# Optimization experiments

Measured on AMD Instinct MI355X. Metric: run time of the kernel, lower is better.

The kernel has to match this reference:

```python
import jax, jax.numpy as jnp
import numpy as np

EPS = 1e-20  # MaskSoftmax epsilon
S, T, B, H, V = 64, 64, 128, 1024, 32000


def _attn(s, h, u, mask, sa_w, sa_b, a1_w, a1_b):
    # Bahdanau attention with mask-softmax over the source (dim 0)
    t = jnp.tanh(s @ sa_w + sa_b + u)               # [S,B,H]
    e = jnp.einsum('sbh,h->sb', t, a1_w) + a1_b     # [S,B]
    x = jnp.exp(e - jnp.max(e, axis=0, keepdims=True)) * mask
    alpha = x / (jnp.sum(x, axis=0, keepdims=True) + EPS)
    return jnp.einsum('sb,sbh->bh', alpha, h)       # [B,H]


def _gru(x, h, ym, W, U, b, C=None, c=None):
    xg = x @ W + b
    if C is not None:
        xg = xg + c @ C
    hg = h @ U
    xz, xr, xh = jnp.split(xg, 3, axis=-1)
    hz, hr, hh = jnp.split(hg, 3, axis=-1)
    z = jax.nn.sigmoid(xz + hz)
    r = jax.nn.sigmoid(xr + hr)
    hn = (1.0 - z) * h + z * jnp.tanh(xh + r * hh)
    m = ym[:, None]
    return m * hn + (1.0 - m) * h


def _forward(ys, xs_h, uh, xs_mask, ys_mask, s_tm1, emb, sa_w, sa_b, a1_w, a1_b,
             ha_w, ha_b, W1, U1, b1, W2, U2, C2, b2,
             ua1_w, ua1_b, ua2_w, ua2_b, ls_w, ls_b, ly_w, ly_b, lc_w, lc_b):
    ys_e = emb[ys]                                              # [T,B,H]
    btg_uh = jnp.einsum('sbh,hk->sbk', xs_h, ha_w) + ha_b        # [S,B,H]

    def step(s, inp):
        y_e, ym = inp
        s_above = _gru(y_e, s, ym, W1, U1, b1)                   # gru1
        a1 = _attn(s_above, xs_h, uh, xs_mask, sa_w, sa_b, a1_w, a1_b)
        a2 = _attn(s_above, xs_h, btg_uh, xs_mask, sa_w, sa_b, a1_w, a1_b)
        s_t = _gru(a1, s_above, ym, W2, U2, b2, C2, a2)          # gru2 with extra ctx
        g = jax.nn.sigmoid(a1 @ ua1_w + ua1_b + a2 @ ua2_w + ua2_b)
        att = g * a1 + (1.0 - g) * a2                            # gated fusion
        logit = s_t @ ls_w + ls_b + y_e @ ly_w + ly_b + att @ lc_w + lc_b  # [B,2H]
        logit = jnp.max(logit.reshape(logit.shape[0], -1, 2), axis=-1)     # maxout
        return s_t, logit

    _, logits = jax.lax.scan(step, s_tm1, (ys_e, ys_mask))       # [T,B,H]
    return logits * ys_mask[:, :, None]


def setup_inputs():
    key = jax.random.key(0)
    ks = jax.random.split(key, 20)
    rn = lambda k, sh, s=0.02: jax.random.normal(k, sh, jnp.float32) * s
    inp = {}
    inp['ys'] = jax.random.randint(ks[0], (T, B), 0, V)
    inp['xs_h'] = jax.random.normal(ks[1], (S, B, H), jnp.float32)
    inp['uh'] = jax.random.normal(ks[2], (S, B, H), jnp.float32)
    inp['xs_mask'] = jnp.ones((S, B), jnp.float32)
    inp['ys_mask'] = jnp.ones((T, B), jnp.float32)
    inp['s_tm1'] = rn(ks[3], (B, H), 1.0)
    emb = rn(ks[4], (V, H), 1.0)
    inp['emb'] = emb.at[0].set(0.0)  # padding_idx = 0
    inp['sa_w'] = rn(ks[5], (H, H)); inp['sa_b'] = jnp.zeros((H,), jnp.float32)
    inp['a1_w'] = rn(ks[6], (H,));   inp['a1_b'] = jnp.zeros((), jnp.float32)
    inp['ha_w'] = rn(ks[7], (H, H)); inp['ha_b'] = jnp.zeros((H,), jnp.float32)
    inp['W1'] = rn(ks[8], (H, 3 * H)); inp['U1'] = rn(ks[9], (H, 3 * H)); inp['b1'] = jnp.zeros((3 * H,), jnp.float32)
    inp['W2'] = rn(ks[10], (H, 3 * H)); inp['U2'] = rn(ks[11], (H, 3 * H)); inp['C2'] = rn(ks[12], (H, 3 * H)); inp['b2'] = jnp.zeros((3 * H,), jnp.float32)
    inp['ua1_w'] = rn(ks[13], (H, H)); inp['ua1_b'] = jnp.zeros((H,), jnp.float32)
    inp['ua2_w'] = rn(ks[14], (H, H)); inp['ua2_b'] = jnp.zeros((H,), jnp.float32)
    inp['ls_w'] = rn(ks[15], (H, 2 * H)); inp['ls_b'] = jnp.zeros((2 * H,), jnp.float32)
    inp['ly_w'] = rn(ks[16], (H, 2 * H)); inp['ly_b'] = jnp.zeros((2 * H,), jnp.float32)
    inp['lc_w'] = rn(ks[17], (H, 2 * H)); inp['lc_b'] = jnp.zeros((2 * H,), jnp.float32)
    return inp


def reference(ys, xs_h, uh, xs_mask, ys_mask, s_tm1, emb, sa_w, sa_b, a1_w, a1_b,
              ha_w, ha_b, W1, U1, b1, W2, U2, C2, b2,
              ua1_w, ua1_b, ua2_w, ua2_b, ls_w, ls_b, ly_w, ly_b, lc_w, lc_b):
    return _forward(ys, xs_h, uh, xs_mask, ys_mask, s_tm1, emb, sa_w, sa_b, a1_w, a1_b,
                    ha_w, ha_b, W1, U1, b1, W2, U2, C2, b2,
                    ua1_w, ua1_b, ua2_w, ua2_b, ls_w, ls_b, ly_w, ly_b, lc_w, lc_b)
```

## Files before the change

### kernel.cpp

```cpp
#include <hip/hip_runtime.h>
#include <hip/hip_bf16.h>
#include <cstddef>
#include <cstdint>

#define Sdim 64
#define Tdim 64
#define Bdim 128
#define Hdim 1024
#define H3 3072
#define TB (Tdim * Bdim)
#define SB (Sdim * Bdim)
#define NWG 256

typedef __attribute__((ext_vector_type(4))) float f32x4;
typedef __attribute__((ext_vector_type(8))) short bf16x8;

__device__ __forceinline__ float rcpf(float x) { return __builtin_amdgcn_rcpf(x); }
__device__ __forceinline__ float sigf(float x) { return rcpf(1.0f + __expf(-x)); }
__device__ __forceinline__ float tanh_fast(float x) {
  x = fminf(fmaxf(x, -15.0f), 15.0f);
  float t = __expf(2.0f * x);
  return (t - 1.0f) * rcpf(t + 1.0f);
}
__device__ __forceinline__ float bl(uint32_t u) { return __uint_as_float(u << 16); }
__device__ __forceinline__ float bh(uint32_t u) { return __uint_as_float(u & 0xffff0000u); }
__device__ __forceinline__ float b2f(uint16_t v) { return __uint_as_float((uint32_t)v << 16); }
__device__ __forceinline__ uint16_t f2b(float f) {
  __hip_bfloat16 h = __float2bfloat16(f);
  return *reinterpret_cast<uint16_t*>(&h);
}

__device__ __forceinline__ uint32_t ald32(const void* p) {
  return __hip_atomic_load((const uint32_t*)p, __ATOMIC_RELAXED, __HIP_MEMORY_SCOPE_AGENT);
}
__device__ __forceinline__ unsigned long long ald64(const void* p) {
  return __hip_atomic_load((const unsigned long long*)p, __ATOMIC_RELAXED, __HIP_MEMORY_SCOPE_AGENT);
}
__device__ __forceinline__ void ast32(void* p, uint32_t v) {
  __hip_atomic_store((uint32_t*)p, v, __ATOMIC_RELAXED, __HIP_MEMORY_SCOPE_AGENT);
}
__device__ __forceinline__ void ast64(void* p, unsigned long long v) {
  __hip_atomic_store((unsigned long long*)p, v, __ATOMIC_RELAXED, __HIP_MEMORY_SCOPE_AGENT);
}
__device__ __forceinline__ float aldf(const void* p) { return __uint_as_float(ald32(p)); }
__device__ __forceinline__ void astf(void* p, float v) { ast32(p, __float_as_uint(v)); }
__device__ __forceinline__ uint4 ald128(const void* p) {
  unsigned long long a = ald64(p);
  unsigned long long b = ald64((const char*)p + 8);
  uint4 r;
  r.x = (uint32_t)a; r.y = (uint32_t)(a >> 32);
  r.z = (uint32_t)b; r.w = (uint32_t)(b >> 32);
  return r;
}
#define PK2(x, y) ((unsigned long long)__float_as_uint(x) | ((unsigned long long)__float_as_uint(y) << 32))
__device__ __forceinline__ float ulo(unsigned long long u) { return __uint_as_float((uint32_t)u); }
__device__ __forceinline__ float uhi(unsigned long long u) { return __uint_as_float((uint32_t)(u >> 32)); }

struct MDesc {
  const uint16_t* A0; const uint16_t* B0;
  const uint16_t* A1; const uint16_t* B1;
  const uint16_t* A2; const uint16_t* B2;
  const float* bias0; const float* bias1; const float* bias2;
  float* C;
  int M, N, K;
};

template<int BM, int BN, int MODE>
__global__ __launch_bounds__(256) void mgemm(MDesc d, const float* __restrict__ ymask,
                                             float* __restrict__ outp)
{
  const int nb = blockIdx.x * BN;
  const int mb = blockIdx.y * BM;
  if (nb >= d.N || mb >= d.M) return;

  __shared__ char lds[(BM + BN) * 128];
  char* As = lds;
  char* Bs = lds + BM * 128;

  const int t = threadIdx.x;
  const int lane = t & 63;
  const int wid = t >> 6;
  const int wm = wid >> 1, wn = wid & 1;
  constexpr int WM = BM / 2, WN = BN / 2;
  constexpr int MR = WM / 16, NR = WN / 16;
  constexpr int CA = BM / 32;
  constexpr int CB = BN / 32;

  const int arow_base = wm * WM + (lane & 15);
  const int brow_base = wn * WN + (lane & 15);
  const int akb = (lane >> 4) * 16;
  const int axA = (arow_base & 7) << 4;
  const int axB = (brow_base & 7) << 4;

  f32x4 acc[MR][NR];
  #pragma unroll
  for (int m = 0; m < MR; ++m)
    #pragma unroll
    for (int n = 0; n < NR; ++n)
      acc[m][n] = (f32x4){0.f, 0.f, 0.f, 0.f};

  const int K = d.K;
  const int nkt = K / 64;

  #pragma unroll 1
  for (int p = 0; p < 3; ++p) {
    const uint16_t* A = (p == 0) ? d.A0 : (p == 1 ? d.A1 : d.A2);
    const uint16_t* B = (p == 0) ? d.B0 : (p == 1 ? d.B1 : d.B2);
    if (A == nullptr) break;

    const char* gA[CA]; int lA[CA];
    const char* gB[CB]; int lB[CB];
    #pragma unroll
    for (int c = 0; c < CA; ++c) {
      int i = c * 256 + t, row = i >> 3, kb = (i & 7) * 16;
      gA[c] = (const char*)A + (size_t)(mb + row) * K * 2 + kb;
      lA[c] = row * 128 + (kb ^ ((row & 7) << 4));
    }
    #pragma unroll
    for (int c = 0; c < CB; ++c) {
      int i = c * 256 + t, row = i >> 3, kb = (i & 7) * 16;
      gB[c] = (const char*)B + (size_t)(nb + row) * K * 2 + kb;
      lB[c] = row * 128 + (kb ^ ((row & 7) << 4));
    }

    uint4 ra[CA], rb[CB];
    #pragma unroll
    for (int c = 0; c < CA; ++c) ra[c] = *(const uint4*)gA[c];
    #pragma unroll
    for (int c = 0; c < CB; ++c) rb[c] = *(const uint4*)gB[c];

    for (int kk = 0; kk < nkt; ++kk) {
      __syncthreads();
      #pragma unroll
      for (int c = 0; c < CA; ++c) *(uint4*)(As + lA[c]) = ra[c];
      #pragma unroll
      for (int c = 0; c < CB; ++c) *(uint4*)(Bs + lB[c]) = rb[c];
      __syncthreads();
      if (kk + 1 < nkt) {
        #pragma unroll
        for (int c = 0; c < CA; ++c) ra[c] = *(const uint4*)(gA[c] + (size_t)(kk + 1) * 128);
        #pragma unroll
        for (int c = 0; c < CB; ++c) rb[c] = *(const uint4*)(gB[c] + (size_t)(kk + 1) * 128);
      }
      #pragma unroll
      for (int ks = 0; ks < 2; ++ks) {
        bf16x8 av[MR], bv[NR];
        #pragma unroll
        for (int m = 0; m < MR; ++m) {
          int row = arow_base + m * 16;
          av[m] = *(const bf16x8*)(As + row * 128 + ((ks * 64 + akb) ^ axA));
        }
        #pragma unroll
        for (int n = 0; n < NR; ++n) {
          int row = brow_base + n * 16;
          bv[n] = *(const bf16x8*)(Bs + row * 128 + ((ks * 64 + akb) ^ axB));
        }
        #pragma unroll
        for (int m = 0; m < MR; ++m)
          #pragma unroll
          for (int n = 0; n < NR; ++n)
            acc[m][n] = __builtin_amdgcn_mfma_f32_16x16x32_bf16(av[m], bv[n], acc[m][n], 0, 0, 0);
      }
    }
  }

  const int cm = (lane >> 4) * 4;
  const int cn = lane & 15;
  #pragma unroll
  for (int n = 0; n < NR; ++n) {
    int col = nb + wn * WN + n * 16 + cn;
    float bias = 0.f;
    if (d.bias0) bias += d.bias0[col];
    if (d.bias1) bias += d.bias1[col];
    if (d.bias2) bias += d.bias2[col];
    #pragma unroll
    for (int m = 0; m < MR; ++m) {
      #pragma unroll
      for (int j = 0; j < 4; ++j) {
        int row = mb + wm * WM + m * 16 + cm + j;
        float v = acc[m][n][j] + bias;
        if (MODE == 1) {
          ((uint16_t*)d.C)[(size_t)row * d.N + col] = f2b(v);
        } else {
          float o = __shfl_xor(v, 1);
          if (!(lane & 1))
            outp[(size_t)row * (d.N / 2) + (col >> 1)] = fmaxf(v, o) * ymask[row];
        }
      }
    }
  }
}

static inline MDesc mk(const uint16_t* A0, const uint16_t* B0,
                       const uint16_t* A1, const uint16_t* B1,
                       const uint16_t* A2, const uint16_t* B2,
                       const float* b0, const float* b1, const float* b2,
                       float* C, int M, int N, int K)
{
  MDesc d;
  d.A0 = A0; d.B0 = B0; d.A1 = A1; d.B1 = B1; d.A2 = A2; d.B2 = B2;
  d.bias0 = b0; d.bias1 = b1; d.bias2 = b2;
  d.C = C; d.M = M; d.N = N; d.K = K;
  return d;
}

__global__ __launch_bounds__(256) void transpose_bf16_k(const float* __restrict__ in,
                                                        uint16_t* __restrict__ out,
                                                        int K, int N)
{
  __shared__ float tile[32][33];
  int nx = blockIdx.x * 32, ky = blockIdx.y * 32;
  int tx = threadIdx.x & 31, ty = threadIdx.x >> 5;
  #pragma unroll
  for (int i = 0; i < 4; ++i)
    tile[ty + i * 8][tx] = in[(size_t)(ky + ty + i * 8) * N + nx + tx];
  __syncthreads();
  #pragma unroll
  for (int i = 0; i < 4; ++i)
    out[(size_t)(nx + ty + i * 8) * K + ky + tx] = f2b(tile[tx][ty + i * 8]);
}

__global__ __launch_bounds__(256) void ptranspose_k(const float* __restrict__ in,
                                                    uint16_t* __restrict__ out,
                                                    int K, int N)
{
  __shared__ float tile[32][33];
  int nx = blockIdx.x * 32, ky = blockIdx.y * 32;
  int tx = threadIdx.x & 31, ty = threadIdx.x >> 5;
  #pragma unroll
  for (int i = 0; i < 4; ++i)
    tile[ty + i * 8][tx] = in[(size_t)(ky + ty + i * 8) * N + nx + tx];
  __syncthreads();
  #pragma unroll
  for (int i = 0; i < 4; ++i) {
    int n = nx + ty + i * 8;
    int h = n & 1023, g = n >> 10;
    int np = (h >> 4) * 48 + g * 16 + (h & 15);
    out[(size_t)np * K + ky + tx] = f2b(tile[tx][ty + i * 8]);
  }
}

__global__ __launch_bounds__(256) void pack_k(const float* __restrict__ b1,
                                              const float* __restrict__ b2,
                                              float* __restrict__ b1p,
                                              float* __restrict__ b2p,
                                              int* __restrict__ bar)
{
  int i = blockIdx.x * 256 + threadIdx.x;
  if (i < 1024) bar[i] = 0;
  if (i < H3) {
    int g = (i >> 4) % 3, hblk = i / 48, hi = i & 15;
    int n = g * 1024 + hblk * 16 + hi;
    b1p[i] = b1[n];
    b2p[i] = b2[n];
  }
}

__global__ __launch_bounds__(256) void cvt_bf16_k(const float* __restrict__ in,
                                                  uint16_t* __restrict__ out)
{
  int gid = blockIdx.x * 256 + threadIdx.x;
  float4 v = ((const float4*)in)[gid];
  uint2 o;
  o.x = (uint32_t)f2b(v.x) | ((uint32_t)f2b(v.y) << 16);
  o.y = (uint32_t)f2b(v.z) | ((uint32_t)f2b(v.w) << 16);
  ((uint2*)out)[gid] = o;
}

__global__ __launch_bounds__(256) void embed_k(const int* __restrict__ ys,
                                               const float* __restrict__ emb,
                                               uint16_t* __restrict__ ys_e)
{
  int gid = blockIdx.x * 256 + threadIdx.x;
  int h4 = gid & 255;
  int tb = gid >> 8;
  int tok = ys[tb];
  float4 v = ((const float4*)emb)[(size_t)tok * 256 + h4];
  uint2 o;
  o.x = (uint32_t)f2b(v.x) | ((uint32_t)f2b(v.y) << 16);
  o.y = (uint32_t)f2b(v.z) | ((uint32_t)f2b(v.w) << 16);
  ((uint2*)ys_e)[gid] = o;
}

struct ScanArgs {
  const uint16_t *U1p, *W2p, *C2p, *U2p;
  const uint16_t *sawt, *ua1t, *ua2t;
  const uint16_t *xw1p;
  const uint16_t *uh_bf, *btg_bf, *xs_bf;
  const uint16_t *stm1_bf;
  const float *s_tm1, *ys_mask, *xs_mask, *a1w, *a1b, *sa_b;
  const float *b2p, *ua1_b, *ua2_b;
  float *sf0, *sf1, *sab_f, *qbuf, *e1, *e2, *c1f, *c2f, *ahg;
  float *p1part, *p5part;
  uint16_t *sab_bf, *c1b, *c2b, *shist_bf, *att_bf;
  int *bar;
};

__device__ __forceinline__ void gsync(int* bar, int gen, int wg) {
  __syncthreads();
  if (threadIdx.x == 0) {
    asm volatile("s_waitcnt vmcnt(0)" ::: "memory");
    int old = __hip_atomic_fetch_add(bar + (wg & 15) * 32, 1,
                                     __ATOMIC_RELAXED, __HIP_MEMORY_SCOPE_AGENT);
    if (old == gen * 16 - 1) {
      int ro = __hip_atomic_fetch_add(bar + 512, 1,
                                      __ATOMIC_RELAXED, __HIP_MEMORY_SCOPE_AGENT);
      if (ro == gen * 16 - 1)
        __hip_atomic_store(bar + 544, gen, __ATOMIC_RELAXED, __HIP_MEMORY_SCOPE_AGENT);
    }
    while (__hip_atomic_load(bar + 544, __ATOMIC_RELAXED, __HIP_MEMORY_SCOPE_AGENT) < gen)
      __builtin_amdgcn_s_sleep(2);
    asm volatile("s_waitcnt vmcnt(0)" ::: "memory");
  }
  __syncthreads();
}

#define STRCACHE 131072
#define HS1 16384
#define HS2 12288
#define HS6 16384


__global__ __launch_bounds__(256, 1) void scan2_k(ScanArgs a) {
  extern __shared__ char lds[];
  char* stg = lds + STRCACHE;
  const int wg = blockIdx.x;
  const int t = threadIdx.x;
  const int lane = t & 63, w = t >> 6;
  const int r15 = lane & 15;
  const int akb = (lane >> 4) * 16;
  int gen = 0;

  float wv[16];
  {
    const float* wp = a.a1w + lane * 16;
    #pragma unroll
    for (int j = 0; j < 16; ++j) wv[j] = wp[j];
  }
  const float abv = a.a1b[0];

  const int b34 = wg & 127;
  const uint16_t* src34 = (wg < 128) ? a.uh_bf : a.btg_bf;
  float* cf34 = (wg < 128) ? a.c1f : a.c2f;
  uint16_t* cb34 = (wg < 128) ? a.c1b : a.c2b;
  const uint16_t* xp34 = a.xs_bf + (size_t)b34 * 1024 + t * 4;

  {
    #pragma unroll
    for (int c = 0; c < 32; ++c) {
      int idx = c * 256 + t;
      int s = idx >> 7, hc = idx & 127;
      const uint16_t* gp = src34 + ((size_t)(s * Bdim + b34)) * 1024 + hc * 8;
      *(uint4*)(lds + s * 2048 + hc * 16) = *(const uint4*)gp;
    }
    __syncthreads();
  }

  const int bh6 = (wg & 127) >> 6, hb6 = wg & 63;
  const char* ga6[4]; int la6[4];
  {
    #pragma unroll
    for (int c = 0; c < 4; ++c) {
      int i = c * 256 + t;
      int row = i >> 3, kb = (i & 7) * 16;
      if (i < 512) {
        ga6[c] = (const char*)a.sab_bf + ((size_t)(bh6 * 64 + row) * 1024) * 2 + kb;
      } else if (i < 896) {
        int j2 = i - 512; int row2 = j2 >> 3;
        ga6[c] = (const char*)a.U2p + ((size_t)(hb6 * 48 + row2) * 1024) * 2 + kb;
        row = 64 + row2;
      } else {
        ga6[c] = (const char*)a.U2p + kb;
      }
      la6[c] = row * 128 + (kb ^ ((row & 7) << 4));
    }
  }

  const int bh5 = (wg & 127) >> 6, hblk = wg & 63;
  const int pairid = wg & 127;
  const int koff = (wg < 128) ? 0 : 8;

  const char* ga5[8]; int la5[8];
  {
    #pragma unroll
    for (int c = 0; c < 8; ++c) {
      int i = c * 256 + t;
      int kb = (i & 7) * 16, grow = i >> 3;
      const char* gp;
      if (grow < 64)       gp = (const char*)a.c1b  + ((size_t)(bh5 * 64 + grow)        * 1024) * 2;
      else if (grow < 128) gp = (const char*)a.c2b  + ((size_t)(bh5 * 64 + grow - 64)   * 1024) * 2;
      else if (grow < 176) gp = (const char*)a.W2p  + ((size_t)(hblk * 48 + grow - 128) * 1024) * 2;
      else if (grow < 224) gp = (const char*)a.C2p  + ((size_t)(hblk * 48 + grow - 176) * 1024) * 2;
      else if (grow < 240) gp = (const char*)a.ua1t + ((size_t)(hblk * 16 + grow - 224) * 1024) * 2;
      else                 gp = (const char*)a.ua2t + ((size_t)(hblk * 16 + grow - 240) * 1024) * 2;
      ga5[c] = gp + kb + (size_t)koff * 128;
      la5[c] = grow * 128 + (kb ^ ((grow & 7) << 4));
    }
  }

  unsigned long long* p1p = (unsigned long long*)a.p1part + (size_t)pairid * 1536 + t;
  unsigned long long* p5p = (unsigned long long*)a.p5part + (size_t)pairid * 2048 + t;

  for (int step = 0; step < Tdim; ++step) {
    const uint16_t* sprev_bf = step ? (a.shist_bf + (size_t)(step - 1) * Bdim * Hdim) : a.stm1_bf;
    const float* sprev_f = (step == 0) ? a.s_tm1 : ((step & 1) ? a.sf0 : a.sf1);
    float* snext_f = (step & 1) ? a.sf1 : a.sf0;
    const float* ymt = a.ys_mask + (size_t)step * Bdim;
    uint16_t* shist_t = a.shist_bf + (size_t)step * Bdim * Hdim;
    uint16_t* att_t = a.att_bf + (size_t)step * Bdim * Hdim;
    const uint16_t* xw1t = a.xw1p + (size_t)step * Bdim * H3;

    {
      const char* ga1[4]; int la1[4];
      #pragma unroll
      for (int c = 0; c < 4; ++c) {
        int i = c * 256 + t;
        int row = i >> 3, kb = (i & 7) * 16;
        if (i < 512) {
          ga1[c] = (const char*)sprev_bf + ((size_t)(bh5 * 64 + row) * 1024) * 2 + kb;
        } else if (i < 896) {
          int j2 = i - 512; int row2 = j2 >> 3;
          ga1[c] = (const char*)a.U1p + ((size_t)(hblk * 48 + row2) * 1024) * 2 + kb;
          row = 64 + row2;
        } else {
          ga1[c] = (const char*)a.U1p + kb;
        }
        ga1[c] += (size_t)koff * 128;
        la1[c] = row * 128 + (kb ^ ((row & 7) << 4));
      }
      f32x4 ac0 = {0.f,0.f,0.f,0.f}, ac1 = ac0, ac2 = ac0;
      const int arow = w * 16 + r15;
      const int axA = (arow & 7) << 4;
      const int axB = (r15 & 7) << 4;
      uint4 rA[4], rB[4];
      auto ld1 = [&](uint4* r, int tile) {
        #pragma unroll
        for (int c = 0; c < 4; ++c)
          r[c] = (c < 2) ? ald128(ga1[c] + (size_t)tile * 128)
                         : *(const uint4*)(ga1[c] + (size_t)tile * 128);
      };
      auto st1 = [&](const uint4* r, int half) {
        char* base = stg + half * HS1;
        #pragma unroll
        for (int c = 0; c < 4; ++c) *(uint4*)(base + la1[c]) = r[c];
      };
      auto cp1 = [&](int half) {
        const char* base = stg + half * HS1;
        #pragma unroll
        for (int ks = 0; ks < 2; ++ks) {
          int ko = ks * 64 + akb;
          bf16x8 av = *(const bf16x8*)(base + arow * 128 + (ko ^ axA));
          bf16x8 b0 = *(const bf16x8*)(base + (64 + r15) * 128 + (ko ^ axB));
          bf16x8 b1 = *(const bf16x8*)(base + (80 + r15) * 128 + (ko ^ axB));
          bf16x8 b2 = *(const bf16x8*)(base + (96 + r15) * 128 + (ko ^ axB));
          ac0 = __builtin_amdgcn_mfma_f32_16x16x32_bf16(av, b0, ac0, 0, 0, 0);
          ac1 = __builtin_amdgcn_mfma_f32_16x16x32_bf16(av, b1, ac1, 0, 0, 0);
          ac2 = __builtin_amdgcn_mfma_f32_16x16x32_bf16(av, b2, ac2, 0, 0, 0);
        }
      };
      ld1(rA, 0); ld1(rB, 1);
      st1(rA, 0);
      #pragma unroll 1
      for (int kk2 = 0; kk2 < 4; ++kk2) {
        __syncthreads();
        st1(rB, 1);
        if (kk2 < 3) ld1(rA, 2 * kk2 + 2);
        cp1(0);
        __syncthreads();
        if (kk2 < 3) { st1(rA, 0); ld1(rB, 2 * kk2 + 3); }
        cp1(1);
      }
      if (wg >= 128) {
        ast64(p1p +    0, PK2(ac0[0], ac0[1]));
        ast64(p1p +  256, PK2(ac0[2], ac0[3]));
        ast64(p1p +  512, PK2(ac1[0], ac1[1]));
        ast64(p1p +  768, PK2(ac1[2], ac1[3]));
        ast64(p1p + 1024, PK2(ac2[0], ac2[1]));
        ast64(p1p + 1280, PK2(ac2[2], ac2[3]));
        __syncthreads();
        if (t == 0)
          __hip_atomic_store(a.bar + 600 + pairid, step + 1,
                             __ATOMIC_RELAXED, __HIP_MEMORY_SCOPE_AGENT);
      } else {
        if (t == 0) {
          while (__hip_atomic_load(a.bar + 600 + pairid,
                                   __ATOMIC_RELAXED, __HIP_MEMORY_SCOPE_AGENT) < step + 1)
            __builtin_amdgcn_s_sleep(1);
        }
        __syncthreads();
        unsigned long long u0 = ald64(p1p), u1 = ald64(p1p + 256),
                           u2 = ald64(p1p + 512), u3 = ald64(p1p + 768),
                           u4 = ald64(p1p + 1024), u5 = ald64(p1p + 1280);
        ac0[0] += ulo(u0); ac0[1] += uhi(u0); ac0[2] += ulo(u1); ac0[3] += uhi(u1);
        ac1[0] += ulo(u2); ac1[1] += uhi(u2); ac1[2] += ulo(u3); ac1[3] += uhi(u3);
        ac2[0] += ulo(u4); ac2[1] += uhi(u4); ac2[2] += ulo(u5); ac2[3] += uhi(u5);
        const int hgl = hblk * 16 + r15;
        const int bbase = bh5 * 64 + w * 16 + ((lane >> 4) << 2);
        #pragma unroll
        for (int j = 0; j < 4; ++j) {
          int b = bbase + j;
          size_t xr_ = (size_t)b * H3 + hblk * 48 + r15;
          float xz = b2f(xw1t[xr_]);
          float xr = b2f(xw1t[xr_ + 16]);
          float xh = b2f(xw1t[xr_ + 32]);
          float hp = aldf(sprev_f + b * 1024 + hgl);
          float z = sigf(xz + ac0[j]);
          float r = sigf(xr + ac1[j]);
          float hn = (1.f - z) * hp + z * tanh_fast(xh + r * ac2[j]);
          float m = ymt[b];
          float o = m * hn + (1.f - m) * hp;
          astf(a.sab_f + b * 1024 + hgl, o);
          uint32_t me = f2b(o);
          uint32_t other = (uint32_t)__shfl_xor((int)me, 1);
          if (!(lane & 1))
            ast32((char*)a.sab_bf + ((size_t)b * 1024 + hgl) * 2, me | (other << 16));
        }
      }
    }
    gsync(a.bar, ++gen, wg);

    if (wg < 64) {
      const int bh2 = wg >> 5, nblk = wg & 31;
      const char* ga2[3]; int la2[3];
      #pragma unroll
      for (int c = 0; c < 3; ++c) {
        int i = c * 256 + t;
        int row, kb = (i & 7) * 16;
        if (i < 512) {
          row = i >> 3;
          ga2[c] = (const char*)a.sab_bf + ((size_t)(bh2 * 64 + row) * 1024) * 2 + kb;
        } else {
          int j2 = i - 512; int row2 = j2 >> 3;
          ga2[c] = (const char*)a.sawt + ((size_t)(nblk * 32 + row2) * 1024) * 2 + kb;
          row = 64 + row2;
        }
        la2[c] = row * 128 + (kb ^ ((row & 7) << 4));
      }
      f32x4 q0 = {0.f,0.f,0.f,0.f}, q1 = q0;
      const int arow = w * 16 + r15;
      const int axA = (arow & 7) << 4;
      const int axB = (r15 & 7) << 4;
      uint4 rA[3], rB[3];
      auto ld2 = [&](uint4* r, int tile) {
        #pragma unroll
        for (int c = 0; c < 3; ++c)
          r[c] = (c < 2) ? ald128(ga2[c] + (size_t)tile * 128)
                         : *(const uint4*)(ga2[c] + (size_t)tile * 128);
      };
      auto st2 = [&](const uint4* r, int half) {
        char* base = stg + half * HS2;
        #pragma unroll
        for (int c = 0; c < 3; ++c) *(uint4*)(base + la2[c]) = r[c];
      };
      auto cp2 = [&](int half) {
        const char* base = stg + half * HS2;
        #pragma unroll
        for (int ks = 0; ks < 2; ++ks) {
          int ko = ks * 64 + akb;
          bf16x8 av = *(const bf16x8*)(base + arow * 128 + (ko ^ axA));
          bf16x8 b0 = *(const bf16x8*)(base + (64 + r15) * 128 + (ko ^ axB));
          bf16x8 b1 = *(const bf16x8*)(base + (80 + r15) * 128 + (ko ^ axB));
          q0 = __builtin_amdgcn_mfma_f32_16x16x32_bf16(av, b0, q0, 0, 0, 0);
          q1 = __builtin_amdgcn_mfma_f32_16x16x32_bf16(av, b1, q1, 0, 0, 0);
        }
      };
      ld2(rA, 0); ld2(rB, 1);
      st2(rA, 0);
      #pragma unroll 1
      for (int kk2 = 0; kk2 < 8; ++kk2) {
        __syncthreads();
        st2(rB, 1);
        if (kk2 < 7) ld2(rA, 2 * kk2 + 2);
        cp2(0);
        __syncthreads();
        if (kk2 < 7) { st2(rA, 0); ld2(rB, 2 * kk2 + 3); }
        cp2(1);
      }
      #pragma unroll
      for (int n = 0; n < 2; ++n) {
        int col = nblk * 32 + n * 16 + r15;
        float sb = a.sa_b[col];
        #pragma unroll
        for (int j = 0; j < 4; ++j) {
          int b = bh2 * 64 + w * 16 + ((lane >> 4) << 2) + j;
          astf(a.qbuf + b * 1024 + col, (n ? q1[j] : q0[j]) + sb);
        }
      }
    } else if (wg >= 128) {
      f32x4 ac0 = {0.f,0.f,0.f,0.f}, ac1 = ac0, ac2 = ac0;
      const int arow = w * 16 + r15;
      const int axA = (arow & 7) << 4;
      const int axB = (r15 & 7) << 4;
      uint4 rA[4], rB[4];
      auto ld6 = [&](uint4* r, int tile) {
        #pragma unroll
        for (int c = 0; c < 4; ++c)
          r[c] = (c < 2) ? ald128(ga6[c] + (size_t)tile * 128)
                         : *(const uint4*)(ga6[c] + (size_t)tile * 128);
      };
      auto st6 = [&](const uint4* r, int half) {
        char* base = stg + half * HS6;
        #pragma unroll
        for (int c = 0; c < 4; ++c) *(uint4*)(base + la6[c]) = r[c];
      };
      auto cp6 = [&](int half) {
        const char* base = stg + half * HS6;
        #pragma unroll
        for (int ks = 0; ks < 2; ++ks) {
          int ko = ks * 64 + akb;
          bf16x8 av = *(const bf16x8*)(base + arow * 128 + (ko ^ axA));
          bf16x8 b0 = *(const bf16x8*)(base + (64 + r15) * 128 + (ko ^ axB));
          bf16x8 b1 = *(const bf16x8*)(base + (80 + r15) * 128 + (ko ^ axB));
          bf16x8 b2 = *(const bf16x8*)(base + (96 + r15) * 128 + (ko ^ axB));
          ac0 = __builtin_amdgcn_mfma_f32_16x16x32_bf16(av, b0, ac0, 0, 0, 0);
          ac1 = __builtin_amdgcn_mfma_f32_16x16x32_bf16(av, b1, ac1, 0, 0, 0);
          ac2 = __builtin_amdgcn_mfma_f32_16x16x32_bf16(av, b2, ac2, 0, 0, 0);
        }
      };
      ld6(rA, 0); ld6(rB, 1);
      st6(rA, 0);
      #pragma unroll 1
      for (int kk2 = 0; kk2 < 8; ++kk2) {
        __syncthreads();
        st6(rB, 1);
        if (kk2 < 7) ld6(rA, 2 * kk2 + 2);
        cp6(0);
        __syncthreads();
        if (kk2 < 7) { st6(rA, 0); ld6(rB, 2 * kk2 + 3); }
        cp6(1);
      }
      const int bbase6 = bh6 * 64 + w * 16 + ((lane >> 4) << 2);
      #pragma unroll
      for (int j = 0; j < 4; ++j) {
        int b = bbase6 + j;
        float* ap = a.ahg + (size_t)b * H3 + hb6 * 48 + r15;
        astf(ap, ac0[j]);
        astf(ap + 16, ac1[j]);
        astf(ap + 32, ac2[j]);
      }
    }
    gsync(a.bar, ++gen, wg);

    {
      float* e_lds = (float*)stg;
      float qv[16];
      const float* qp = a.qbuf + (size_t)b34 * 1024 + lane * 16;
      #pragma unroll
      for (int k2 = 0; k2 < 8; ++k2) {
        unsigned long long q2 = ald64(qp + k2 * 2);
        qv[2 * k2]     = __uint_as_float((uint32_t)q2);
        qv[2 * k2 + 1] = __uint_as_float((uint32_t)(q2 >> 32));
      }
      #pragma unroll 1
      for (int si = 0; si < 16; ++si) {
        int srow = w * 16 + si;
        const char* cpp = lds + srow * 2048 + lane * 32;
        uint4 u0 = *(const uint4*)cpp;
        uint4 u1 = *(const uint4*)(cpp + 16);
        float pv = 0.f;
        uint32_t uu[8] = {u0.x,u0.y,u0.z,u0.w,u1.x,u1.y,u1.z,u1.w};
        #pragma unroll
        for (int k = 0; k < 8; ++k) {
          pv += wv[2*k]   * tanh_fast(qv[2*k]   + bl(uu[k]));
          pv += wv[2*k+1] * tanh_fast(qv[2*k+1] + bh(uu[k]));
        }
        #pragma unroll
        for (int off = 32; off > 0; off >>= 1) pv += __shfl_xor(pv, off);
        if (lane == 0) e_lds[srow] = pv + abv;
      }
      __syncthreads();
      if (w == 0) {
        float vv = e_lds[lane];
        float mx = vv;
        #pragma unroll
        for (int off = 32; off > 0; off >>= 1) mx = fmaxf(mx, __shfl_xor(mx, off));
        float x = __expf(vv - mx) * a.xs_mask[lane * Bdim + b34];
        float sm = x;
        #pragma unroll
        for (int off = 32; off > 0; off >>= 1) sm += __shfl_xor(sm, off);
        e_lds[lane] = x * rcpf(sm + 1e-20f);
      }
      __syncthreads();
      float s0 = 0.f, s1 = 0.f, s2 = 0.f, s3 = 0.f;
      #pragma unroll 8
      for (int s = 0; s < Sdim; ++s) {
        unsigned long long u = *(const unsigned long long*)(xp34 + (size_t)s * Bdim * 1024);
        float aa = e_lds[s];
        s0 += aa * bl((uint32_t)u);
        s1 += aa * bh((uint32_t)u);
        s2 += aa * bl((uint32_t)(u >> 32));
        s3 += aa * bh((uint32_t)(u >> 32));
      }
      size_t o = (size_t)b34 * 1024 + t * 4;
      ast64(cf34 + o,     (unsigned long long)__float_as_uint(s0)
                        | ((unsigned long long)__float_as_uint(s1) << 32));
      ast64(cf34 + o + 2, (unsigned long long)__float_as_uint(s2)
                        | ((unsigned long long)__float_as_uint(s3) << 32));
      unsigned long long pb = (unsigned long long)f2b(s0)
                            | ((unsigned long long)f2b(s1) << 16)
                            | ((unsigned long long)f2b(s2) << 32)
                            | ((unsigned long long)f2b(s3) << 48);
      ast64((char*)cb34 + o * 2, pb);
    }
    uint4 v5w[8];
    {
      #pragma unroll
      for (int c = 4; c < 8; ++c) {
        v5w[c - 4] = *(const uint4*)ga5[c];
        v5w[c]     = *(const uint4*)(ga5[c] + 128);
      }
    }
    gsync(a.bar, ++gen, wg);

    {
      f32x4 ax0 = {0.f,0.f,0.f,0.f}, ax1 = ax0, ax2 = ax0, ag = ax0;
      uint4 rA[8], rB[8];
      auto ld5 = [&](uint4* r, int tile) {
        #pragma unroll
        for (int c = 0; c < 8; ++c)
          r[c] = (c < 4) ? ald128(ga5[c] + (size_t)tile * 128)
                         : *(const uint4*)(ga5[c] + (size_t)tile * 128);
      };
      auto st5 = [&](const uint4* r) {
        #pragma unroll
        for (int c = 0; c < 8; ++c) *(uint4*)(stg + la5[c]) = r[c];
      };
      auto cp5 = [&]() {
        const char* base = stg;
        #pragma unroll
        for (int ks = 0; ks < 2; ++ks) {
          const int ko = ks * 64 + akb;
          #define LD(row_) (*(const bf16x8*)(base + (row_) * 128 + (ko ^ (((row_) & 7) << 4))))
          bf16x8 a1v = LD(w * 16 + r15);
          bf16x8 a2v = LD(64 + w * 16 + r15);
          bf16x8 bw0 = LD(128 + r15), bw1 = LD(144 + r15), bw2 = LD(160 + r15);
          bf16x8 bc0 = LD(176 + r15), bc1 = LD(192 + r15), bc2 = LD(208 + r15);
          bf16x8 g1v = LD(224 + r15), g2v = LD(240 + r15);
          #undef LD
          ax0 = __builtin_amdgcn_mfma_f32_16x16x32_bf16(a1v, bw0, ax0, 0, 0, 0);
          ax0 = __builtin_amdgcn_mfma_f32_16x16x32_bf16(a2v, bc0, ax0, 0, 0, 0);
          ax1 = __builtin_amdgcn_mfma_f32_16x16x32_bf16(a1v, bw1, ax1, 0, 0, 0);
          ax1 = __builtin_amdgcn_mfma_f32_16x16x32_bf16(a2v, bc1, ax1, 0, 0, 0);
          ax2 = __builtin_amdgcn_mfma_f32_16x16x32_bf16(a1v, bw2, ax2, 0, 0, 0);
          ax2 = __builtin_amdgcn_mfma_f32_16x16x32_bf16(a2v, bc2, ax2, 0, 0, 0);
          ag  = __builtin_amdgcn_mfma_f32_16x16x32_bf16(a1v, g1v, ag, 0, 0, 0);
          ag  = __builtin_amdgcn_mfma_f32_16x16x32_bf16(a2v, g2v, ag, 0, 0, 0);
        }
      };
      #pragma unroll
      for (int c = 0; c < 4; ++c) {
        rA[c] = ald128(ga5[c]);
        rB[c] = ald128(ga5[c] + 128);
      }
      #pragma unroll
      for (int c = 4; c < 8; ++c) { rA[c] = v5w[c - 4]; rB[c] = v5w[c]; }
      #pragma unroll 1
      for (int k2 = 0; k2 < 4; ++k2) {
        __syncthreads();
        st5(rA);
        __syncthreads();
        if (k2 < 3) ld5(rA, 2 * k2 + 2);
        cp5();
        __syncthreads();
        st5(rB);
        __syncthreads();
        if (k2 < 3) ld5(rB, 2 * k2 + 3);
        cp5();
      }
      if (wg >= 128) {
        ast64(p5p +    0, PK2(ax0[0], ax0[1]));
        ast64(p5p +  256, PK2(ax0[2], ax0[3]));
        ast64(p5p +  512, PK2(ax1[0], ax1[1]));
        ast64(p5p +  768, PK2(ax1[2], ax1[3]));
        ast64(p5p + 1024, PK2(ax2[0], ax2[1]));
        ast64(p5p + 1280, PK2(ax2[2], ax2[3]));
        ast64(p5p + 1536, PK2(ag[0], ag[1]));
        ast64(p5p + 1792, PK2(ag[2], ag[3]));
        __syncthreads();
        if (t == 0)
          __hip_atomic_store(a.bar + 728 + pairid, step + 1,
                             __ATOMIC_RELAXED, __HIP_MEMORY_SCOPE_AGENT);
      } else {
        if (t == 0) {
          while (__hip_atomic_load(a.bar + 728 + pairid,
                                   __ATOMIC_RELAXED, __HIP_MEMORY_SCOPE_AGENT) < step + 1)
            __builtin_amdgcn_s_sleep(1);
        }
        __syncthreads();
        unsigned long long u0 = ald64(p5p), u1 = ald64(p5p + 256),
                           u2 = ald64(p5p + 512), u3 = ald64(p5p + 768),
                           u4 = ald64(p5p + 1024), u5 = ald64(p5p + 1280),
                           u6 = ald64(p5p + 1536), u7 = ald64(p5p + 1792);
        ax0[0] += ulo(u0); ax0[1] += uhi(u0); ax0[2] += ulo(u1); ax0[3] += uhi(u1);
        ax1[0] += ulo(u2); ax1[1] += uhi(u2); ax1[2] += ulo(u3); ax1[3] += uhi(u3);
        ax2[0] += ulo(u4); ax2[1] += uhi(u4); ax2[2] += ulo(u5); ax2[3] += uhi(u5);
        ag[0]  += ulo(u6); ag[1]  += uhi(u6); ag[2]  += ulo(u7); ag[3]  += uhi(u7);
        const int hgl = hblk * 16 + r15;
        float bz  = a.b2p[hblk * 48 + r15];
        float brr = a.b2p[hblk * 48 + 16 + r15];
        float bhh = a.b2p[hblk * 48 + 32 + r15];
        float gb  = a.ua1_b[hgl] + a.ua2_b[hgl];
        const int bbase = bh5 * 64 + w * 16 + ((lane >> 4) << 2);
        float ahz[4], ahr[4], ahh[4], hpv[4], c1v[4], c2v[4];
        #pragma unroll
        for (int j = 0; j < 4; ++j) {
          int b = bbase + j;
          const float* ap = a.ahg + (size_t)b * H3 + hblk * 48 + r15;
          ahz[j] = aldf(ap);
          ahr[j] = aldf(ap + 16);
          ahh[j] = aldf(ap + 32);
          hpv[j] = aldf(a.sab_f + (size_t)b * 1024 + hgl);
          c1v[j] = aldf(a.c1f + (size_t)b * 1024 + hgl);
          c2v[j] = aldf(a.c2f + (size_t)b * 1024 + hgl);
        }
        #pragma unroll
        for (int j = 0; j < 4; ++j) {
          int b = bbase + j;
          float hp = hpv[j];
          float z = sigf(ax0[j] + bz + ahz[j]);
          float r = sigf(ax1[j] + brr + ahr[j]);
          float hn = (1.f - z) * hp + z * tanh_fast(ax2[j] + bhh + r * ahh[j]);
          float m = ymt[b];
          float st = m * hn + (1.f - m) * hp;
          astf(snext_f + b * 1024 + hgl, st);
          uint32_t me = f2b(st);
          uint32_t other = (uint32_t)__shfl_xor((int)me, 1);
          if (!(lane & 1))
            ast32((char*)shist_t + ((size_t)b * 1024 + hgl) * 2, me | (other << 16));
          float g = sigf(ag[j] + gb);
          float att = g * c1v[j] + (1.f - g) * c2v[j];
          att_t[(size_t)b * 1024 + hgl] = f2b(att);
        }
      }
    }
    gsync(a.bar, ++gen, wg);
  }
}

extern "C" void kernel_launch(void* const* d_in, const int* in_sizes, int n_in,
                              void* d_out, int out_size, void* d_ws, size_t ws_size,
                              hipStream_t stream)
{
  const int*   ys      = (const int*)  d_in[0];
  const float* xs_h    = (const float*)d_in[1];
  const float* uh      = (const float*)d_in[2];
  const float* xs_mask = (const float*)d_in[3];
  const float* ys_mask = (const float*)d_in[4];
  const float* s_tm1   = (const float*)d_in[5];
  const float* emb     = (const float*)d_in[6];
  const float* sa_w    = (const float*)d_in[7];
  const float* sa_b    = (const float*)d_in[8];
  const float* a1_w    = (const float*)d_in[9];
  const float* a1_b    = (const float*)d_in[10];
  const float* ha_w    = (const float*)d_in[11];
  const float* ha_b    = (const float*)d_in[12];
  const float* W1      = (const float*)d_in[13];
  const float* U1      = (const float*)d_in[14];
  const float* b1      = (const float*)d_in[15];
  const float* W2      = (const float*)d_in[16];
  const float* U2      = (const float*)d_in[17];
  const float* C2      = (const float*)d_in[18];
  const float* b2      = (const float*)d_in[19];
  const float* ua1_w   = (const float*)d_in[20];
  const float* ua1_b   = (const float*)d_in[21];
  const float* ua2_w   = (const float*)d_in[22];
  const float* ua2_b   = (const float*)d_in[23];
  const float* ls_w    = (const float*)d_in[24];
  const float* ls_b    = (const float*)d_in[25];
  const float* ly_w    = (const float*)d_in[26];
  const float* ly_b    = (const float*)d_in[27];
  const float* lc_w    = (const float*)d_in[28];
  const float* lc_b    = (const float*)d_in[29];
  (void)in_sizes; (void)n_in; (void)out_size; (void)ws_size;

  float* out = (float*)d_out;

  char* wp = (char*)d_ws;
  auto alloc = [&](size_t bytes) { char* r = wp; wp += (bytes + 255) & ~(size_t)255; return r; };

  uint16_t* W1p  = (uint16_t*)alloc((size_t)H3 * Hdim * 2);
  uint16_t* U1p  = (uint16_t*)alloc((size_t)H3 * Hdim * 2);
  uint16_t* W2p  = (uint16_t*)alloc((size_t)H3 * Hdim * 2);
  uint16_t* U2p  = (uint16_t*)alloc((size_t)H3 * Hdim * 2);
  uint16_t* C2p  = (uint16_t*)alloc((size_t)H3 * Hdim * 2);
  uint16_t* sawt = (uint16_t*)alloc((size_t)Hdim * Hdim * 2);
  uint16_t* hawt = (uint16_t*)alloc((size_t)Hdim * Hdim * 2);
  uint16_t* ua1t = (uint16_t*)alloc((size_t)Hdim * Hdim * 2);
  uint16_t* ua2t = (uint16_t*)alloc((size_t)Hdim * Hdim * 2);
  uint16_t* lst  = (uint16_t*)alloc((size_t)2048 * Hdim * 2);
  uint16_t* lyt  = (uint16_t*)alloc((size_t)2048 * Hdim * 2);
  uint16_t* lct  = (uint16_t*)alloc((size_t)2048 * Hdim * 2);
  float* b1p = (float*)alloc((size_t)H3 * 4);
  float* b2p = (float*)alloc((size_t)H3 * 4);
  int* bar   = (int*)alloc(4096);
  uint16_t* uh_bf   = (uint16_t*)alloc((size_t)SB * Hdim * 2);
  uint16_t* xs_bf   = (uint16_t*)alloc((size_t)SB * Hdim * 2);
  uint16_t* btg_bf  = (uint16_t*)alloc((size_t)SB * Hdim * 2);
  uint16_t* ys_e_bf = (uint16_t*)alloc((size_t)TB * Hdim * 2);
  uint16_t* xw1p    = (uint16_t*)alloc((size_t)TB * H3 * 2);
  uint16_t* shist_bf= (uint16_t*)alloc((size_t)TB * Hdim * 2);
  uint16_t* att_bf  = (uint16_t*)alloc((size_t)TB * Hdim * 2);
  uint16_t* stm1_bf = (uint16_t*)alloc((size_t)Bdim * Hdim * 2);
  float* sab_f = (float*)alloc((size_t)Bdim * Hdim * 4);
  uint16_t* sab_bf = (uint16_t*)alloc((size_t)Bdim * Hdim * 2);
  float* qbuf = (float*)alloc((size_t)Bdim * Hdim * 4);
  float* c1f  = (float*)alloc((size_t)Bdim * Hdim * 4);
  float* c2f  = (float*)alloc((size_t)Bdim * Hdim * 4);
  uint16_t* c1b = (uint16_t*)alloc((size_t)Bdim * Hdim * 2);
  uint16_t* c2b = (uint16_t*)alloc((size_t)Bdim * Hdim * 2);
  float* e1 = (float*)alloc((size_t)SB * 4);
  float* e2 = (float*)alloc((size_t)SB * 4);
  float* sf0 = (float*)alloc((size_t)Bdim * Hdim * 4);
  float* sf1 = (float*)alloc((size_t)Bdim * Hdim * 4);
  float* ahg = (float*)alloc((size_t)Bdim * H3 * 4);
  float* p1part = (float*)alloc((size_t)128 * 1536 * 8);
  float* p5part = (float*)alloc((size_t)128 * 2048 * 8);

  pack_k<<<12, 256, 0, stream>>>(b1, b2, b1p, b2p, bar);

  auto ptr3 = [&](const float* in, uint16_t* o) {
    ptranspose_k<<<dim3(H3 / 32, Hdim / 32), 256, 0, stream>>>(in, o, Hdim, H3);
  };
  ptr3(W1, W1p); ptr3(U1, U1p); ptr3(W2, W2p); ptr3(U2, U2p); ptr3(C2, C2p);

  auto tr = [&](const float* in, uint16_t* o, int K, int N) {
    transpose_bf16_k<<<dim3(N / 32, K / 32), 256, 0, stream>>>(in, o, K, N);
  };
  tr(sa_w, sawt, Hdim, Hdim); tr(ha_w, hawt, Hdim, Hdim);
  tr(ua1_w, ua1t, Hdim, Hdim); tr(ua2_w, ua2t, Hdim, Hdim);
  tr(ls_w, lst, Hdim, 2048); tr(ly_w, lyt, Hdim, 2048); tr(lc_w, lct, Hdim, 2048);

  cvt_bf16_k<<<(SB * Hdim / 4) / 256, 256, 0, stream>>>(uh, uh_bf);
  cvt_bf16_k<<<(SB * Hdim / 4) / 256, 256, 0, stream>>>(xs_h, xs_bf);
  cvt_bf16_k<<<(Bdim * Hdim / 4) / 256, 256, 0, stream>>>(s_tm1, stm1_bf);
  embed_k<<<(TB * Hdim / 4) / 256, 256, 0, stream>>>(ys, emb, ys_e_bf);

  {
    MDesc d = mk(ys_e_bf, W1p, 0, 0, 0, 0, b1p, 0, 0, (float*)xw1p, TB, H3, Hdim);
    mgemm<128, 128, 1><<<dim3(H3 / 128, TB / 128), 256, 0, stream>>>(d, nullptr, nullptr);
  }
  {
    MDesc d = mk(xs_bf, hawt, 0, 0, 0, 0, ha_b, 0, 0, (float*)btg_bf, SB, Hdim, Hdim);
    mgemm<128, 128, 1><<<dim3(Hdim / 128, SB / 128), 256, 0, stream>>>(d, nullptr, nullptr);
  }

  static bool attr_set = false;
  if (!attr_set) {
    hipFuncSetAttribute((const void*)scan2_k,
                        hipFuncAttributeMaxDynamicSharedMemorySize, 163840);
    attr_set = true;
  }
  ScanArgs sa;
  sa.U1p = U1p; sa.W2p = W2p; sa.C2p = C2p; sa.U2p = U2p;
  sa.sawt = sawt; sa.ua1t = ua1t; sa.ua2t = ua2t;
  sa.xw1p = xw1p;
  sa.uh_bf = uh_bf; sa.btg_bf = btg_bf; sa.xs_bf = xs_bf;
  sa.stm1_bf = stm1_bf;
  sa.s_tm1 = s_tm1; sa.ys_mask = ys_mask; sa.xs_mask = xs_mask;
  sa.a1w = a1_w; sa.a1b = a1_b; sa.sa_b = sa_b;
  sa.b2p = b2p; sa.ua1_b = ua1_b; sa.ua2_b = ua2_b;
  sa.sf0 = sf0; sa.sf1 = sf1; sa.sab_f = sab_f; sa.qbuf = qbuf;
  sa.e1 = e1; sa.e2 = e2; sa.c1f = c1f; sa.c2f = c2f; sa.ahg = ahg;
  sa.p1part = p1part; sa.p5part = p5part;
  sa.sab_bf = sab_bf; sa.c1b = c1b; sa.c2b = c2b;
  sa.shist_bf = shist_bf; sa.att_bf = att_bf;
  sa.bar = bar;
  scan2_k<<<NWG, 256, 163840, stream>>>(sa);

  {
    MDesc d = mk(shist_bf, lst, ys_e_bf, lyt, att_bf, lct, ls_b, ly_b, lc_b,
                 nullptr, TB, 2048, Hdim);
    mgemm<128, 128, 2><<<dim3(2048 / 128, TB / 128), 256, 0, stream>>>(d, ys_mask, out);
  }
}
```

Measured before the change: 4.893 ms.

## Split sa_w query GEMM across 128 workgroups, double-buffer stage-5 LDS, reload attention sources

The per-step query projection (s_above @ sa_w) was computed by 64 workgroups. It is now split along K across 128 workgroups, with the upper half writing partial sums to a new buffer and signalling through a per-pair flag that the lower half spins on before reducing. The stage-5 GEMM loop now double-buffers between two LDS regions, which cuts the __syncthreads per tile from four to two. The attention source layout in LDS is changed to interleave 16-byte chunks into two 1 KB halves, and the LDS copy of the source rows is reloaded at the end of each step because the LDS is now reused as a second staging buffer. Risks include spin-wait latency on the flags and extra global reloads of source data every step.

```diff
diff --git a/kernel.cpp b/kernel.cpp
--- a/kernel.cpp
+++ b/kernel.cpp
@@ -290,8 +290,8 @@
   const uint16_t *stm1_bf;
   const float *s_tm1, *ys_mask, *xs_mask, *a1w, *a1b, *sa_b;
   const float *b2p, *ua1_b, *ua2_b;
-  float *sf0, *sf1, *sab_f, *qbuf, *e1, *e2, *c1f, *c2f, *ahg;
-  float *p1part, *p5part;
+  float *sf0, *sf1, *sab_f, *qbuf, *c1f, *c2f, *ahg;
+  float *p1part, *p5part, *p2part;
   uint16_t *sab_bf, *c1b, *c2b, *shist_bf, *att_bf;
   int *bar;
 };
@@ -351,7 +351,7 @@
       int idx = c * 256 + t;
       int s = idx >> 7, hc = idx & 127;
       const uint16_t* gp = src34 + ((size_t)(s * Bdim + b34)) * 1024 + hc * 8;
-      *(uint4*)(lds + s * 2048 + hc * 16) = *(const uint4*)gp;
+      *(uint4*)(lds + s * 2048 + (hc & 1) * 1024 + (hc >> 1) * 16) = *(const uint4*)gp;
     }
     __syncthreads();
   }
@@ -380,6 +380,10 @@
   const int pairid = wg & 127;
   const int koff = (wg < 128) ? 0 : 8;
 
+  const int p2id = wg & 63;
+  const int bh2 = p2id >> 5, nblk = p2id & 31;
+  const int koff2 = (wg >= 64 && wg < 128) ? 8 : 0;
+
   const char* ga5[8]; int la5[8];
   {
     #pragma unroll
@@ -400,6 +404,7 @@
 
   unsigned long long* p1p = (unsigned long long*)a.p1part + (size_t)pairid * 1536 + t;
   unsigned long long* p5p = (unsigned long long*)a.p5part + (size_t)pairid * 2048 + t;
+  unsigned long long* p2p = (unsigned long long*)a.p2part + (size_t)p2id * 1024 + t;
 
   for (int step = 0; step < Tdim; ++step) {
     const uint16_t* sprev_bf = step ? (a.shist_bf + (size_t)(step - 1) * Bdim * Hdim) : a.stm1_bf;
@@ -519,8 +524,7 @@
     }
     gsync(a.bar, ++gen, wg);
 
-    if (wg < 64) {
-      const int bh2 = wg >> 5, nblk = wg & 31;
+    if (wg < 128) {
       const char* ga2[3]; int la2[3];
       #pragma unroll
       for (int c = 0; c < 3; ++c) {
@@ -534,6 +538,7 @@
           ga2[c] = (const char*)a.sawt + ((size_t)(nblk * 32 + row2) * 1024) * 2 + kb;
           row = 64 + row2;
         }
+        ga2[c] += (size_t)koff2 * 128;
         la2[c] = row * 128 + (kb ^ ((row & 7) << 4));
       }
       f32x4 q0 = {0.f,0.f,0.f,0.f}, q1 = q0;
@@ -567,26 +572,47 @@
       ld2(rA, 0); ld2(rB, 1);
       st2(rA, 0);
       #pragma unroll 1
-      for (int kk2 = 0; kk2 < 8; ++kk2) {
+      for (int kk2 = 0; kk2 < 4; ++kk2) {
         __syncthreads();
         st2(rB, 1);
-        if (kk2 < 7) ld2(rA, 2 * kk2 + 2);
+        if (kk2 < 3) ld2(rA, 2 * kk2 + 2);
         cp2(0);
         __syncthreads();
-        if (kk2 < 7) { st2(rA, 0); ld2(rB, 2 * kk2 + 3); }
+        if (kk2 < 3) { st2(rA, 0); ld2(rB, 2 * kk2 + 3); }
         cp2(1);
       }
-      #pragma unroll
-      for (int n = 0; n < 2; ++n) {
-        int col = nblk * 32 + n * 16 + r15;
-        float sb = a.sa_b[col];
-        #pragma unroll
-        for (int j = 0; j < 4; ++j) {
-          int b = bh2 * 64 + w * 16 + ((lane >> 4) << 2) + j;
-          astf(a.qbuf + b * 1024 + col, (n ? q1[j] : q0[j]) + sb);
-        }
-      }
-    } else if (wg >= 128) {
+      if (wg >= 64) {
+        ast64(p2p +   0, PK2(q0[0], q0[1]));
+        ast64(p2p + 256, PK2(q0[2], q0[3]));
+        ast64(p2p + 512, PK2(q1[0], q1[1]));
+        ast64(p2p + 768, PK2(q1[2], q1[3]));
+        __syncthreads();
+        if (t == 0)
+          __hip_atomic_store(a.bar + 856 + p2id, step + 1,
+                             __ATOMIC_RELAXED, __HIP_MEMORY_SCOPE_AGENT);
+      } else {
+        if (t == 0) {
+          while (__hip_atomic_load(a.bar + 856 + p2id,
+                                   __ATOMIC_RELAXED, __HIP_MEMORY_SCOPE_AGENT) < step + 1)
+            __builtin_amdgcn_s_sleep(1);
+        }
+        __syncthreads();
+        unsigned long long u0 = ald64(p2p), u1 = ald64(p2p + 256),
+                           u2 = ald64(p2p + 512), u3 = ald64(p2p + 768);
+        q0[0] += ulo(u0); q0[1] += uhi(u0); q0[2] += ulo(u1); q0[3] += uhi(u1);
+        q1[0] += ulo(u2); q1[1] += uhi(u2); q1[2] += ulo(u3); q1[3] += uhi(u3);
+        #pragma unroll
+        for (int n = 0; n < 2; ++n) {
+          int col = nblk * 32 + n * 16 + r15;
+          float sb = a.sa_b[col];
+          #pragma unroll
+          for (int j = 0; j < 4; ++j) {
+            int b = bh2 * 64 + w * 16 + ((lane >> 4) << 2) + j;
+            astf(a.qbuf + b * 1024 + col, (n ? q1[j] : q0[j]) + sb);
+          }
+        }
+      }
+    } else {
       f32x4 ac0 = {0.f,0.f,0.f,0.f}, ac1 = ac0, ac2 = ac0;
       const int arow = w * 16 + r15;
       const int axA = (arow & 7) << 4;
@@ -654,13 +680,18 @@
       #pragma unroll 1
       for (int si = 0; si < 16; ++si) {
         int srow = w * 16 + si;
-        const char* cpp = lds + srow * 2048 + lane * 32;
-        uint4 u0 = *(const uint4*)cpp;
-        uint4 u1 = *(const uint4*)(cpp + 16);
+        const char* rowp = lds + srow * 2048 + lane * 16;
+        uint4 u0 = *(const uint4*)rowp;
+        uint4 u1 = *(const uint4*)(rowp + 1024);
         float pv = 0.f;
         uint32_t uu[8] = {u0.x,u0.y,u0.z,u0.w,u1.x,u1.y,u1.z,u1.w};
         #pragma unroll
-        for (int k = 0; k < 8; ++k) {
+        for (int k = 0; k < 4; ++k) {
+          pv += wv[2*k]   * tanh_fast(qv[2*k]   + bl(uu[k]));
+          pv += wv[2*k+1] * tanh_fast(qv[2*k+1] + bh(uu[k]));
+        }
+        #pragma unroll
+        for (int k = 4; k < 8; ++k) {
           pv += wv[2*k]   * tanh_fast(qv[2*k]   + bl(uu[k]));
           pv += wv[2*k+1] * tanh_fast(qv[2*k+1] + bh(uu[k]));
         }
@@ -721,12 +752,13 @@
           r[c] = (c < 4) ? ald128(ga5[c] + (size_t)tile * 128)
                          : *(const uint4*)(ga5[c] + (size_t)tile * 128);
       };
-      auto st5 = [&](const uint4* r) {
-        #pragma unroll
-        for (int c = 0; c < 8; ++c) *(uint4*)(stg + la5[c]) = r[c];
-      };
-      auto cp5 = [&]() {
-        const char* base = stg;
+      auto st5 = [&](const uint4* r, int half) {
+        char* base = half ? lds : stg;
+        #pragma unroll
+        for (int c = 0; c < 8; ++c) *(uint4*)(base + la5[c]) = r[c];
+      };
+      auto cp5 = [&](int half) {
+        const char* base = half ? lds : stg;
         #pragma unroll
         for (int ks = 0; ks < 2; ++ks) {
           const int ko = ks * 64 + akb;
@@ -754,18 +786,16 @@
       }
       #pragma unroll
       for (int c = 4; c < 8; ++c) { rA[c] = v5w[c - 4]; rB[c] = v5w[c]; }
+      st5(rA, 0);
       #pragma unroll 1
-      for (int k2 = 0; k2 < 4; ++k2) {
-        __syncthreads();
-        st5(rA);
-        __syncthreads();
-        if (k2 < 3) ld5(rA, 2 * k2 + 2);
-        cp5();
-        __syncthreads();
-        st5(rB);
-        __syncthreads();
-        if (k2 < 3) ld5(rB, 2 * k2 + 3);
-        cp5();
+      for (int kk2 = 0; kk2 < 4; ++kk2) {
+        __syncthreads();
+        st5(rB, 1);
+        if (kk2 < 3) ld5(rA, 2 * kk2 + 2);
+        cp5(0);
+        __syncthreads();
+        if (kk2 < 3) { st5(rA, 0); ld5(rB, 2 * kk2 + 3); }
+        cp5(1);
       }
       if (wg >= 128) {
         ast64(p5p +    0, PK2(ax0[0], ax0[1]));
@@ -831,6 +861,13 @@
           float att = g * c1v[j] + (1.f - g) * c2v[j];
           att_t[(size_t)b * 1024 + hgl] = f2b(att);
         }
+      }
+      #pragma unroll
+      for (int c = 0; c < 8; ++c) {
+        int idx = c * 256 + t;
+        int s = idx >> 7, hc = idx & 127;
+        const uint16_t* gp = src34 + ((size_t)(s * Bdim + b34)) * 1024 + hc * 8;
+        *(uint4*)(lds + s * 2048 + (hc & 1) * 1024 + (hc >> 1) * 16) = *(const uint4*)gp;
       }
     }
     gsync(a.bar, ++gen, wg);
@@ -908,13 +945,12 @@
   float* c2f  = (float*)alloc((size_t)Bdim * Hdim * 4);
   uint16_t* c1b = (uint16_t*)alloc((size_t)Bdim * Hdim * 2);
   uint16_t* c2b = (uint16_t*)alloc((size_t)Bdim * Hdim * 2);
-  float* e1 = (float*)alloc((size_t)SB * 4);
-  float* e2 = (float*)alloc((size_t)SB * 4);
   float* sf0 = (float*)alloc((size_t)Bdim * Hdim * 4);
   float* sf1 = (float*)alloc((size_t)Bdim * Hdim * 4);
   float* ahg = (float*)alloc((size_t)Bdim * H3 * 4);
   float* p1part = (float*)alloc((size_t)128 * 1536 * 8);
   float* p5part = (float*)alloc((size_t)128 * 2048 * 8);
+  float* p2part = (float*)alloc((size_t)64 * 1024 * 8);
 
   pack_k<<<12, 256, 0, stream>>>(b1, b2, b1p, b2p, bar);
 
@@ -960,8 +996,8 @@
   sa.a1w = a1_w; sa.a1b = a1_b; sa.sa_b = sa_b;
   sa.b2p = b2p; sa.ua1_b = ua1_b; sa.ua2_b = ua2_b;
   sa.sf0 = sf0; sa.sf1 = sf1; sa.sab_f = sab_f; sa.qbuf = qbuf;
-  sa.e1 = e1; sa.e2 = e2; sa.c1f = c1f; sa.c2f = c2f; sa.ahg = ahg;
-  sa.p1part = p1part; sa.p5part = p5part;
+  sa.c1f = c1f; sa.c2f = c2f; sa.ahg = ahg;
+  sa.p1part = p1part; sa.p5part = p5part; sa.p2part = p2part;
   sa.sab_bf = sab_bf; sa.c1b = c1b; sa.c2b = c2b;
   sa.shist_bf = shist_bf; sa.att_bf = att_bf;
   sa.bar = bar;
```

After: 5.104 ms. +4.3%, slower.
